# Kernel optimization log

Hardware: AMD Instinct MI355X
Metric: run time of the kernel (lower is better)

## Reference

```python
import jax, jax.numpy as jnp
import numpy as np

B, S, D, H = 4, 2048, 512, 8
KD = D // H          # key_dim == head_dim == 64
FFN = 4 * D

def _ln(x, g, b, eps):
    mu = x.mean(-1, keepdims=True)
    var = ((x - mu) ** 2).mean(-1, keepdims=True)
    return (x - mu) / jnp.sqrt(var + eps) * g + b

def setup_inputs():
    key = jax.random.key(0)
    ks = jax.random.split(key, 8)
    def lin(k, o, i, scale=0.02):
        k1, k2 = jax.random.split(k)
        return (jax.random.normal(k1, (o, i), jnp.float32) * scale,
                jax.random.normal(k2, (o,), jnp.float32) * scale)
    wq, bq = lin(ks[0], D, D)
    wk, bk = lin(ks[1], D, D)
    wv, bv = lin(ks[2], D, D)
    wg, bg = lin(ks[3], D, D)
    wo, bo = lin(ks[4], D, D)
    fc1_w, fc1_b = lin(ks[5], FFN, D)
    fc2_w, fc2_b = lin(ks[6], D, FFN)
    return {
        'src': jax.random.normal(ks[7], (B, S, D), jnp.float32),
        'mask': jnp.zeros((S, S), jnp.bool_),
        'padding_mask': jnp.zeros((B, S), jnp.bool_),
        'wq': wq, 'bq': bq, 'wk': wk, 'bk': bk, 'wv': wv, 'bv': bv,
        'wg': wg, 'bg': bg, 'wo': wo, 'bo': bo,
        'fc1_w': fc1_w, 'fc1_b': fc1_b, 'fc2_w': fc2_w, 'fc2_b': fc2_b,
        'ln_ffn_g': jnp.ones((FFN,), jnp.float32), 'ln_ffn_b': jnp.zeros((FFN,), jnp.float32),
        'n0_g': jnp.ones((D,), jnp.float32), 'n0_b': jnp.zeros((D,), jnp.float32),
        'n1_g': jnp.ones((D,), jnp.float32), 'n1_b': jnp.zeros((D,), jnp.float32),
    }

def reference(src, mask, padding_mask, wq, bq, wk, bk, wv, bv, wg, bg, wo, bo,
              fc1_w, fc1_b, fc2_w, fc2_b, ln_ffn_g, ln_ffn_b, n0_g, n0_b, n1_g, n1_b):
    b, s, d = src.shape
    # RetNet per-head decay mask (h, s, s): exp((i-j)*log(gamma_h)) on the lower triangle,
    # row-normalized by sqrt(row sum) (torchscale RetNetRelPos, parallel mode).
    idx = jnp.arange(s)
    diff = (idx[:, None] - idx[None, :]).astype(src.dtype)
    decay = jnp.log(1.0 - 2.0 ** (-5.0 - jnp.arange(H, dtype=src.dtype)))
    dm = jnp.where(diff[None] >= 0, jnp.exp(diff[None] * decay[:, None, None]), 0.0)
    dm = dm / jnp.sqrt(dm.sum(-1, keepdims=True))
    # projections; k scaled by key_dim**-0.5 before head split
    q = (src @ wq.T + bq).reshape(b, s, H, KD).transpose(0, 2, 1, 3)
    k = ((src @ wk.T + bk) * (KD ** -0.5)).reshape(b, s, H, KD).transpose(0, 2, 1, 3)
    v = src @ wv.T + bv
    g = src @ wg.T + bg
    # parallel retention: additive decay bias, detached L1 row normalization
    qk = jnp.einsum('bhid,bhjd->bhij', q, k) + dm[None]
    den = jnp.maximum(jnp.abs(jax.lax.stop_gradient(qk).sum(-1, keepdims=True)), 1.0)
    qk = qk / den
    vr = v.reshape(b, s, H, KD).transpose(0, 2, 1, 3)
    o = jnp.einsum('bhij,bhjd->bhid', qk, vr).transpose(0, 2, 1, 3)  # (b,s,h,hd)
    # per-head LayerNorm, eps=1e-6, no affine
    mu = o.mean(-1, keepdims=True)
    o = (o - mu) / jnp.sqrt(((o - mu) ** 2).mean(-1, keepdims=True) + 1e-6)
    o = jax.nn.silu(g) * o.reshape(b, s, d)
    o = o @ wo.T + bo
    # post-norm residual layout
    x = _ln(src + o, n0_g, n0_b, 1e-5)
    h = jax.nn.gelu(x @ fc1_w.T + fc1_b, approximate=False)
    h = _ln(h, ln_ffn_g, ln_ffn_b, 1e-6)  # subln
    h = h @ fc2_w.T + fc2_b
    return _ln(x + h, n1_g, n1_b, 1e-5)
```

## Files before the change

kernel.cpp:

```cpp
#include <hip/hip_runtime.h>
#include <hip/hip_bf16.h>
#include <math.h>

#define DEV __device__ __forceinline__

typedef __attribute__((ext_vector_type(4))) float f32x4;
typedef __attribute__((ext_vector_type(16))) float f32x16;
typedef __attribute__((ext_vector_type(8))) short bf16x8;
typedef __attribute__((ext_vector_type(8))) unsigned short u16x8;
typedef unsigned short u16;
typedef unsigned int u32;

DEV u16 f2bf(float f) {
  union { float f; u32 u; } v; v.f = f;
  u32 r = v.u + 0x7fffu + ((v.u >> 16) & 1u);
  return (u16)(r >> 16);
}
DEV float bf2f(u16 h) {
  union { u32 u; float f; } v; v.u = ((u32)h) << 16;
  return v.f;
}
DEV float bfel(bf16x8 v, int e) {
  union { bf16x8 b; u16x8 u; } x; x.b = v; return bf2f(x.u[e]);
}

DEV void gl_lds16(const u16* g, u16* s) {
  __builtin_amdgcn_global_load_lds((const __attribute__((address_space(1))) void*)g,
                                   (__attribute__((address_space(3))) void*)s, 16, 0, 0);
}

DEV void barrier_() {
  __builtin_amdgcn_sched_barrier(0);
  asm volatile("" ::: "memory");
  __builtin_amdgcn_s_barrier();
  asm volatile("" ::: "memory");
  __builtin_amdgcn_sched_barrier(0);
}

#define MFMA16(a, b, c) __builtin_amdgcn_mfma_f32_16x16x32_bf16((a), (b), (c), 0, 0, 0)
#define MFMA32(a, b, c) __builtin_amdgcn_mfma_f32_32x32x16_bf16((a), (b), (c), 0, 0, 0)

DEV void cast8(const float* in, u16* out, float s) {
  f32x4 a = *(const f32x4*)in;
  f32x4 b = *(const f32x4*)(in + 4);
  u16x8 r;
  r[0] = f2bf(a[0] * s); r[1] = f2bf(a[1] * s); r[2] = f2bf(a[2] * s); r[3] = f2bf(a[3] * s);
  r[4] = f2bf(b[0] * s); r[5] = f2bf(b[1] * s); r[6] = f2bf(b[2] * s); r[7] = f2bf(b[3] * s);
  *(u16x8*)out = r;
}

__global__ __launch_bounds__(256) void prep_cast(
    const float* __restrict__ src, const float* __restrict__ wq, const float* __restrict__ wk,
    const float* __restrict__ wv, const float* __restrict__ wg, const float* __restrict__ wo,
    const float* __restrict__ fc1, const float* __restrict__ fc2,
    const float* __restrict__ bq, const float* __restrict__ bk,
    const float* __restrict__ bv, const float* __restrict__ bg,
    u16* __restrict__ src_bf, u16* __restrict__ Wcat, u16* __restrict__ wo_bf,
    u16* __restrict__ fc1_bf, u16* __restrict__ fc2_bf, float* __restrict__ bcat) {
  int u = blockIdx.x * 256 + threadIdx.x;
  if (u < 524288) {
    cast8(src + (size_t)u * 8, src_bf + (size_t)u * 8, 1.0f);
  } else if (u < 557056) {
    int v = u - 524288; cast8(wq + (size_t)v * 8, Wcat + (size_t)v * 8, 1.0f);
  } else if (u < 589824) {
    int v = u - 557056; cast8(wk + (size_t)v * 8, Wcat + 262144 + (size_t)v * 8, 0.125f);
  } else if (u < 622592) {
    int v = u - 589824; cast8(wv + (size_t)v * 8, Wcat + 524288 + (size_t)v * 8, 1.0f);
  } else if (u < 655360) {
    int v = u - 622592; cast8(wg + (size_t)v * 8, Wcat + 786432 + (size_t)v * 8, 1.0f);
  } else if (u < 688128) {
    int v = u - 655360; cast8(wo + (size_t)v * 8, wo_bf + (size_t)v * 8, 1.0f);
  } else if (u < 819200) {
    int v = u - 688128; cast8(fc1 + (size_t)v * 8, fc1_bf + (size_t)v * 8, 1.0f);
  } else if (u < 950272) {
    int v = u - 819200; cast8(fc2 + (size_t)v * 8, fc2_bf + (size_t)v * 8, 1.0f);
  } else if (u < 950528) {
    int v = u - 950272;
    #pragma unroll
    for (int e = 0; e < 8; e++) {
      int c = v * 8 + e;
      float val;
      if (c < 512)       val = bq[c];
      else if (c < 1024) val = bk[c - 512] * 0.125f;
      else if (c < 1536) val = bv[c - 1024];
      else               val = bg[c - 1536];
      bcat[c] = val;
    }
  }
}

template <int ACT>
__global__ __launch_bounds__(256) void gemm_v3(
    const u16* __restrict__ A, const u16* __restrict__ W, const float* __restrict__ bias,
    u16* __restrict__ Ob, int N, int K, int TN) {
  __shared__ __align__(16) u16 sm[2][16384];
  const int t = threadIdx.x, l = t & 63;
  const int w = t >> 6, wr = (w >> 1) * 64, wc = (w & 1) * 64;
  const int lc = l & 15, lch = l >> 4;
  const int NT = K >> 6;

  const int orig = blockIdx.x;
  const int cpx = gridDim.x >> 3;
  const int sid = (orig & 7) * cpx + (orig >> 3);
  const int bm = (sid / TN) * 128, bn = (sid % TN) * 128;

  const int srow = t >> 3, sc8 = t & 7;
  const u16* stA = A + (size_t)(bm + srow) * K + ((sc8 ^ (srow & 7)) * 8);
  const u16* stB = W + (size_t)(bn + srow) * K + ((sc8 ^ (srow & 7)) * 8);

#define STAGE(bidx, kt)                                                        \
  {                                                                            \
    u16* d = (u16*)sm[bidx] + t * 8;                                           \
    _Pragma("unroll")                                                          \
    for (int j = 0; j < 4; j++)                                                \
      gl_lds16(stA + (size_t)j * 32 * K + (kt), d + j * 2048);                 \
    _Pragma("unroll")                                                          \
    for (int j = 0; j < 4; j++)                                                \
      gl_lds16(stB + (size_t)j * 32 * K + (kt), d + 8192 + j * 2048);          \
  }

  f32x4 acc[4][4] = {};

  STAGE(0, 0)

  for (int tt = 0; tt < NT; ++tt) {
    if (tt + 1 < NT) {
      STAGE((tt + 1) & 1, (tt + 1) * 64)
      asm volatile("s_waitcnt vmcnt(8)" ::: "memory");
    } else {
      asm volatile("s_waitcnt vmcnt(0)" ::: "memory");
    }
    barrier_();
    const u16* bufp = sm[tt & 1];
    bf16x8 af[4][2], bfv[4][2];
    #pragma unroll
    for (int mi = 0; mi < 4; mi++) {
      const int row = wr + mi * 16 + lc;
      #pragma unroll
      for (int ks = 0; ks < 2; ks++) {
        const int ch = ks * 4 + lch;
        af[mi][ks] = *(const bf16x8*)&bufp[row * 64 + ((ch ^ (row & 7)) * 8)];
      }
    }
    #pragma unroll
    for (int ni = 0; ni < 4; ni++) {
      const int row = wc + ni * 16 + lc;
      #pragma unroll
      for (int ks = 0; ks < 2; ks++) {
        const int ch = ks * 4 + lch;
        bfv[ni][ks] = *(const bf16x8*)&bufp[8192 + row * 64 + ((ch ^ (row & 7)) * 8)];
      }
    }
    #pragma unroll
    for (int ks = 0; ks < 2; ks++)
      #pragma unroll
      for (int mi = 0; mi < 4; mi++)
        #pragma unroll
        for (int ni = 0; ni < 4; ni++)
          acc[mi][ni] = MFMA16(af[mi][ks], bfv[ni][ks], acc[mi][ni]);
    asm volatile("s_waitcnt lgkmcnt(0)" ::: "memory");
    barrier_();
  }
#undef STAGE

  u16* osm = (u16*)sm;
  #pragma unroll
  for (int ni = 0; ni < 4; ni++) {
    const int col = wc + ni * 16 + lc;
    const float bb = bias[bn + col];
    const int ckey = col >> 3, clow = col & 7;
    #pragma unroll
    for (int mi = 0; mi < 4; mi++) {
      #pragma unroll
      for (int r = 0; r < 4; r++) {
        const int row = wr + mi * 16 + lch * 4 + r;
        float v = acc[mi][ni][r] + bb;
        if (ACT == 1) v = 0.5f * v * (1.0f + erff(v * 0.70710678118f));
        osm[row * 128 + ((ckey ^ ((row & 7) << 1)) << 3) + clow] = f2bf(v);
      }
    }
  }
  __syncthreads();
  #pragma unroll
  for (int p = 0; p < 8; p++) {
    const int flat = p * 256 + t;
    const int row = flat >> 4, c = flat & 15;
    u16x8 y = *(const u16x8*)&osm[row * 128 + ((c ^ ((row & 7) << 1)) << 3)];
    *(u16x8*)&Ob[(size_t)(bm + row) * N + bn + c * 8] = y;
  }
}

template <int ACT>
__global__ __launch_bounds__(256) void gemm_m64(
    const u16* __restrict__ A, const u16* __restrict__ W, const float* __restrict__ bias,
    u16* __restrict__ Ob, int N, int K, int TN) {
  __shared__ __align__(16) u16 sm[2][12288];
  const int t = threadIdx.x, l = t & 63;
  const int w = t >> 6, wr = (w >> 1) * 32, wc = (w & 1) * 64;
  const int lc = l & 15, lch = l >> 4;
  const int NT = K >> 6;

  const int orig = blockIdx.x;
  const int cpx = gridDim.x >> 3;
  const int sid = (orig & 7) * cpx + (orig >> 3);
  const int bm = (sid / TN) * 64, bn = (sid % TN) * 128;

  const int srow = t >> 3, sc8 = t & 7;
  const u16* stA = A + (size_t)(bm + srow) * K + ((sc8 ^ (srow & 7)) * 8);
  const u16* stB = W + (size_t)(bn + srow) * K + ((sc8 ^ (srow & 7)) * 8);

#define STAGE(bidx, kt)                                                        \
  {                                                                            \
    u16* d = (u16*)sm[bidx] + t * 8;                                           \
    _Pragma("unroll")                                                          \
    for (int j = 0; j < 2; j++)                                                \
      gl_lds16(stA + (size_t)j * 32 * K + (kt), d + j * 2048);                 \
    _Pragma("unroll")                                                          \
    for (int j = 0; j < 4; j++)                                                \
      gl_lds16(stB + (size_t)j * 32 * K + (kt), d + 4096 + j * 2048);          \
  }

  f32x4 acc[2][4] = {};

  STAGE(0, 0)

  for (int tt = 0; tt < NT; ++tt) {
    if (tt + 1 < NT) {
      STAGE((tt + 1) & 1, (tt + 1) * 64)
      asm volatile("s_waitcnt vmcnt(6)" ::: "memory");
    } else {
      asm volatile("s_waitcnt vmcnt(0)" ::: "memory");
    }
    barrier_();
    const u16* bufp = sm[tt & 1];
    bf16x8 af[2][2], bfv[4][2];
    #pragma unroll
    for (int mi = 0; mi < 2; mi++) {
      const int row = wr + mi * 16 + lc;
      #pragma unroll
      for (int ks = 0; ks < 2; ks++) {
        const int ch = ks * 4 + lch;
        af[mi][ks] = *(const bf16x8*)&bufp[row * 64 + ((ch ^ (row & 7)) * 8)];
      }
    }
    #pragma unroll
    for (int ni = 0; ni < 4; ni++) {
      const int row = wc + ni * 16 + lc;
      #pragma unroll
      for (int ks = 0; ks < 2; ks++) {
        const int ch = ks * 4 + lch;
        bfv[ni][ks] = *(const bf16x8*)&bufp[4096 + row * 64 + ((ch ^ (row & 7)) * 8)];
      }
    }
    #pragma unroll
    for (int ks = 0; ks < 2; ks++)
      #pragma unroll
      for (int mi = 0; mi < 2; mi++)
        #pragma unroll
        for (int ni = 0; ni < 4; ni++)
          acc[mi][ni] = MFMA16(af[mi][ks], bfv[ni][ks], acc[mi][ni]);
    asm volatile("s_waitcnt lgkmcnt(0)" ::: "memory");
    barrier_();
  }
#undef STAGE

  u16* osm = (u16*)sm;
  #pragma unroll
  for (int ni = 0; ni < 4; ni++) {
    const int col = wc + ni * 16 + lc;
    const float bb = bias[bn + col];
    const int ckey = col >> 3, clow = col & 7;
    #pragma unroll
    for (int mi = 0; mi < 2; mi++) {
      #pragma unroll
      for (int r = 0; r < 4; r++) {
        const int row = wr + mi * 16 + lch * 4 + r;
        float v = acc[mi][ni][r] + bb;
        if (ACT == 1) v = 0.5f * v * (1.0f + erff(v * 0.70710678118f));
        osm[row * 128 + ((ckey ^ ((row & 7) << 1)) << 3) + clow] = f2bf(v);
      }
    }
  }
  __syncthreads();
  #pragma unroll
  for (int p = 0; p < 4; p++) {
    const int flat = p * 256 + t;
    const int row = flat >> 4, c = flat & 15;
    u16x8 y = *(const u16x8*)&osm[row * 128 + ((c ^ ((row & 7) << 1)) << 3)];
    *(u16x8*)&Ob[(size_t)(bm + row) * N + bn + c * 8] = y;
  }
}

__global__ __launch_bounds__(256) void transkv(
    const u16* __restrict__ qkvg, u16* __restrict__ ktg, u16* __restrict__ vtg,
    float* __restrict__ Wtab) {
  __shared__ u16 Lk[64 * 72], Lv[64 * 72];
  const int t = threadIdx.x;
  const int bh = blockIdx.x, c = blockIdx.y, b = bh >> 3, h = bh & 7;
  const int jt = c * 64;
  const u16* kptr = qkvg + (size_t)(b * 2048 + jt) * 2048 + 512 + h * 64;
  const u16* vptr = kptr + 512;
  const int r0 = t >> 3, c0 = (t & 7) * 8;
  u16x8 k0 = *(const u16x8*)(kptr + (size_t)r0 * 2048 + c0);
  u16x8 k1 = *(const u16x8*)(kptr + (size_t)(r0 + 32) * 2048 + c0);
  u16x8 v0 = *(const u16x8*)(vptr + (size_t)r0 * 2048 + c0);
  u16x8 v1 = *(const u16x8*)(vptr + (size_t)(r0 + 32) * 2048 + c0);
  #pragma unroll
  for (int e = 0; e < 8; e++) {
    Lk[(c0 + e) * 72 + r0] = k0[e];  Lk[(c0 + e) * 72 + 32 + r0] = k1[e];
    Lv[(c0 + e) * 72 + r0] = v0[e];  Lv[(c0 + e) * 72 + 32 + r0] = v1[e];
  }
  __syncthreads();
  {
    u16* kd = ktg + (size_t)bh * 64 * 2048 + jt;
    u16* vd = vtg + (size_t)bh * 64 * 2048 + jt;
    *(u16x8*)(kd + (size_t)r0 * 2048 + c0)        = *(const u16x8*)&Lk[r0 * 72 + c0];
    *(u16x8*)(kd + (size_t)(r0 + 32) * 2048 + c0) = *(const u16x8*)&Lk[(r0 + 32) * 72 + c0];
    *(u16x8*)(vd + (size_t)r0 * 2048 + c0)        = *(const u16x8*)&Lv[r0 * 72 + c0];
    *(u16x8*)(vd + (size_t)(r0 + 32) * 2048 + c0) = *(const u16x8*)&Lv[(r0 + 32) * 72 + c0];
  }
  if (t < 64) {
    const float gamma = 1.0f - exp2f(-5.0f - (float)h);
    float acc = 0.0f, p = 1.0f;
    for (int jj = 0; jj < 64; jj++) {
      acc += p * bf2f(Lv[t * 72 + (63 - jj)]);
      p *= gamma;
    }
    Wtab[((size_t)bh * 32 + c) * 64 + t] = acc;
  }
}

__global__ __launch_bounds__(256) void scan_kernel(
    const u16* __restrict__ ktg, float* __restrict__ Ctab, float* __restrict__ ksum) {
  __shared__ float ps[4][64];
  const int t = threadIdx.x, bh = blockIdx.x, h = bh & 7;
  const int a = t & 63, q = t >> 6;
  const u16* kr = ktg + (size_t)bh * 64 * 2048 + (size_t)a * 2048 + q * 512;
  float s = 0.0f;
  for (int j = 0; j < 512; j += 8) {
    u16x8 v = *(const u16x8*)(kr + j);
    #pragma unroll
    for (int e = 0; e < 8; e++) s += bf2f(v[e]);
  }
  ps[q][a] = s;
  __syncthreads();
  if (t < 64) {
    ksum[bh * 64 + t] = ps[0][t] + ps[1][t] + ps[2][t] + ps[3][t];
    const float gamma = 1.0f - exp2f(-5.0f - (float)h);
    const float g64 = exp2f(64.0f * log2f(gamma));
    float* Wp = Ctab + (size_t)bh * 32 * 64 + t;
    float C = 0.0f;
    for (int c = 0; c < 32; c++) {
      C = C * g64 + Wp[c * 64];
      Wp[c * 64] = C;
    }
  }
}

__global__ __launch_bounds__(256) void vtk_kernel(
    const u16* __restrict__ vtg, const u16* __restrict__ ktg, u16* __restrict__ vtk) {
  __shared__ float red[3][4096];
  const int t = threadIdx.x, l = t & 63, w = t >> 6;
  const int bh = blockIdx.x;
  const int lc = l & 15, lch = l >> 4;
  const u16* vb = vtg + (size_t)bh * 64 * 2048;
  const u16* kb = ktg + (size_t)bh * 64 * 2048;
  f32x4 acc[4][4] = {};
  for (int it = 0; it < 16; ++it) {
    const int j0 = w * 512 + it * 32 + lch * 8;
    bf16x8 af[4], bfr[4];
    #pragma unroll
    for (int mt = 0; mt < 4; mt++)
      af[mt] = *(const bf16x8*)(vb + (size_t)(mt * 16 + lc) * 2048 + j0);
    #pragma unroll
    for (int nt = 0; nt < 4; nt++)
      bfr[nt] = *(const bf16x8*)(kb + (size_t)(nt * 16 + lc) * 2048 + j0);
    #pragma unroll
    for (int mt = 0; mt < 4; mt++)
      #pragma unroll
      for (int nt = 0; nt < 4; nt++)
        acc[mt][nt] = MFMA16(af[mt], bfr[nt], acc[mt][nt]);
  }
  if (w > 0) {
    #pragma unroll
    for (int mt = 0; mt < 4; mt++)
      #pragma unroll
      for (int nt = 0; nt < 4; nt++)
        #pragma unroll
        for (int r = 0; r < 4; r++)
          red[w - 1][(mt * 16 + lch * 4 + r) * 64 + nt * 16 + lc] = acc[mt][nt][r];
  }
  __syncthreads();
  if (w == 0) {
    u16* out = vtk + (size_t)bh * 64 * 64;
    #pragma unroll
    for (int mt = 0; mt < 4; mt++)
      #pragma unroll
      for (int nt = 0; nt < 4; nt++)
        #pragma unroll
        for (int r = 0; r < 4; r++) {
          int row = mt * 16 + lch * 4 + r, col = nt * 16 + lc;
          float v = acc[mt][nt][r] + red[0][row * 64 + col] + red[1][row * 64 + col] +
                    red[2][row * 64 + col];
          out[row * 64 + col] = f2bf(v);
        }
  }
}

__global__ __launch_bounds__(512) void ret_out(
    const u16* __restrict__ qkvg, const u16* __restrict__ vtg,
    const u16* __restrict__ vtk, const float* __restrict__ Ctab,
    const float* __restrict__ ksum, u16* __restrict__ gated) {
  const int S = 2048, DD = 2048;
  const int bh = blockIdx.x, b = bh >> 3, h = bh & 7;
  const int t = threadIdx.x, l = t & 63, w = t >> 6;
  const int lid = l & 31, hi = l >> 5;
  const int wrow = blockIdx.y * 256 + w * 32;
  const int i_q = wrow + lid;
  const int chunk = wrow >> 6;
  const int iloc = i_q & 63;

  __shared__ __align__(16) u16 sm[18432];
  float* smf = (float*)sm;

  const size_t base = (size_t)b * S * DD + (size_t)h * 64;
  const u16* qp = qkvg + base;
  const u16* gp = qkvg + base + 1536;

  const float gamma = 1.0f - exp2f(-5.0f - (float)h);
  const float l2g = log2f(gamma);
  const float rowsum = (1.0f - exp2f((float)(i_q + 1) * l2g)) * exp2f(5.0f + (float)h);
  const float rrs = rsqrtf(rowsum);

  {
    const int il = t >> 3, j0 = (t & 7) * 8;
    u16x8 row;
    #pragma unroll
    for (int e = 0; e < 8; e++) {
      int d = il - (j0 + e);
      row[e] = (d >= 0) ? f2bf(exp2f((float)d * l2g)) : (u16)0;
    }
    *(u16x8*)&sm[il * 72 + j0] = row;
  }
  if (t < 256) {
    int cc = blockIdx.y * 4 - 1 + (t >> 6);
    smf[4608 + t] = (cc >= 0) ? Ctab[((size_t)bh * 32 + cc) * 64 + (t & 63)] : 0.0f;
  } else if (t < 320) {
    smf[4864 + (t - 256)] = ksum[bh * 64 + (t - 256)];
  }
  __syncthreads();

  bf16x8 qf[4];
  #pragma unroll
  for (int kc = 0; kc < 4; kc++)
    qf[kc] = *(const bf16x8*)(qp + (size_t)i_q * DD + kc * 16 + 8 * hi);

  const u16* vt_b = vtg + (size_t)bh * 64 * S;
  const u16* vk_b = vtk + (size_t)bh * 64 * 64;

  f32x16 accO0, accO1;
  #pragma unroll
  for (int r = 0; r < 16; r++) { accO0[r] = 0.0f; accO1[r] = 0.0f; }

  #pragma unroll
  for (int kc = 0; kc < 4; kc++) {
    bf16x8 lb = *(const bf16x8*)&sm[iloc * 72 + kc * 16 + hi * 8];
    bf16x8 va0 = *(const bf16x8*)(vt_b + (size_t)lid * S + chunk * 64 + kc * 16 + hi * 8);
    bf16x8 va1 = *(const bf16x8*)(vt_b + (size_t)(lid + 32) * S + chunk * 64 + kc * 16 + hi * 8);
    accO0 = MFMA32(va0, lb, accO0);
    accO1 = MFMA32(va1, lb, accO1);
  }
  {
    const float gpw = exp2f((float)(iloc + 1) * l2g);
    const float* Cst = &smf[4608 + (w >> 1) * 64];
    #pragma unroll
    for (int r = 0; r < 16; r++) {
      int br = (r & 3) + 8 * (r >> 2) + 4 * hi;
      accO0[r] += gpw * Cst[br];
      accO1[r] += gpw * Cst[32 + br];
    }
  }
  #pragma unroll
  for (int r = 0; r < 16; r++) { accO0[r] *= rrs; accO1[r] *= rrs; }
  #pragma unroll
  for (int kc = 0; kc < 4; kc++) {
    bf16x8 ka0 = *(const bf16x8*)(vk_b + (size_t)lid * 64 + kc * 16 + hi * 8);
    bf16x8 ka1 = *(const bf16x8*)(vk_b + (size_t)(lid + 32) * 64 + kc * 16 + hi * 8);
    accO0 = MFMA32(ka0, qf[kc], accO0);
    accO1 = MFMA32(ka1, qf[kc], accO1);
  }
  float dsum = 0.0f;
  #pragma unroll
  for (int kc = 0; kc < 4; kc++) {
    const float* Ks = &smf[4864 + kc * 16 + hi * 8];
    #pragma unroll
    for (int e = 0; e < 8; e++) dsum += bfel(qf[kc], e) * Ks[e];
  }
  dsum += __shfl_xor(dsum, 32);
  float den = dsum + sqrtf(rowsum);
  float rden = 1.0f / fmaxf(fabsf(den), 1.0f);

  float o0[16], o1[16];
  float s1 = 0.0f, s2 = 0.0f;
  #pragma unroll
  for (int r = 0; r < 16; r++) {
    o0[r] = accO0[r] * rden; s1 += o0[r]; s2 += o0[r] * o0[r];
    o1[r] = accO1[r] * rden; s1 += o1[r]; s2 += o1[r] * o1[r];
  }
  s1 += __shfl_xor(s1, 32);
  s2 += __shfl_xor(s2, 32);
  float mu = s1 * (1.0f / 64.0f);
  float var = s2 * (1.0f / 64.0f) - mu * mu;
  float rv = rsqrtf(var + 1e-6f);

  __syncthreads();

  u16* Ot = sm + w * 2304;
  #pragma unroll
  for (int r = 0; r < 16; r++) {
    int d = (r & 3) + 8 * (r >> 2) + 4 * hi;
    Ot[lid * 72 + d]      = f2bf((o0[r] - mu) * rv);
    Ot[lid * 72 + 32 + d] = f2bf((o1[r] - mu) * rv);
  }
  {
    const int i2 = l >> 1, half = l & 1;
    const int row = wrow + i2;
    #pragma unroll
    for (int c = 0; c < 4; c++) {
      u16x8 y8 = *(const u16x8*)&Ot[i2 * 72 + half * 32 + c * 8];
      u16x8 g8 = *(const u16x8*)(gp + (size_t)row * DD + half * 32 + c * 8);
      u16x8 o8;
      #pragma unroll
      for (int e = 0; e < 8; e++) {
        float gv = bf2f(g8[e]);
        float sg = gv / (1.0f + __expf(-gv));
        o8[e] = f2bf(bf2f(y8[e]) * sg);
      }
      *(u16x8*)&gated[((size_t)(b * S + row)) * 512 + h * 64 + half * 32 + c * 8] = o8;
    }
  }
}

__global__ __launch_bounds__(256) void add_ln512(
    const float* __restrict__ A, const u16* __restrict__ Bv,
    const float* __restrict__ gam, const float* __restrict__ bet, float eps,
    float* __restrict__ Of, u16* __restrict__ Ob) {
  int row = blockIdx.x * 4 + (threadIdx.x >> 6);
  int l = threadIdx.x & 63;
  const float* a = A + (size_t)row * 512 + l * 8;
  f32x4 a0 = *(const f32x4*)a, a1 = *(const f32x4*)(a + 4);
  u16x8 cv = *(const u16x8*)(Bv + (size_t)row * 512 + l * 8);
  float x[8];
  #pragma unroll
  for (int e = 0; e < 4; e++) { x[e] = a0[e] + bf2f(cv[e]); x[4 + e] = a1[e] + bf2f(cv[4 + e]); }
  float s = 0.f, s2 = 0.f;
  #pragma unroll
  for (int e = 0; e < 8; e++) { s += x[e]; s2 += x[e] * x[e]; }
  #pragma unroll
  for (int m = 1; m <= 32; m <<= 1) { s += __shfl_xor(s, m); s2 += __shfl_xor(s2, m); }
  float mu = s * (1.0f / 512.0f);
  float var = s2 * (1.0f / 512.0f) - mu * mu;
  float rinv = rsqrtf(var + eps);
  f32x4 g0 = *(const f32x4*)(gam + l * 8), g1 = *(const f32x4*)(gam + l * 8 + 4);
  f32x4 b0 = *(const f32x4*)(bet + l * 8), b1 = *(const f32x4*)(bet + l * 8 + 4);
  f32x4 y0, y1;
  #pragma unroll
  for (int e = 0; e < 4; e++) {
    y0[e] = (x[e] - mu) * rinv * g0[e] + b0[e];
    y1[e] = (x[4 + e] - mu) * rinv * g1[e] + b1[e];
  }
  float* op = Of + (size_t)row * 512 + l * 8;
  *(f32x4*)op = y0;
  *(f32x4*)(op + 4) = y1;
  if (Ob) {
    u16x8 rb_;
    #pragma unroll
    for (int e = 0; e < 4; e++) { rb_[e] = f2bf(y0[e]); rb_[4 + e] = f2bf(y1[e]); }
    *(u16x8*)(Ob + (size_t)row * 512 + l * 8) = rb_;
  }
}

__global__ __launch_bounds__(256) void subln_ffn(
    u16* __restrict__ hbuf, const float* __restrict__ gam, const float* __restrict__ bet) {
  int row = blockIdx.x * 4 + (threadIdx.x >> 6);
  int l = threadIdx.x & 63;
  u16* p = hbuf + (size_t)row * 2048;
  float x[32];
  #pragma unroll
  for (int cch = 0; cch < 4; cch++) {
    u16x8 v = *(const u16x8*)(p + cch * 512 + l * 8);
    #pragma unroll
    for (int e = 0; e < 8; e++) x[cch * 8 + e] = bf2f(v[e]);
  }
  float s = 0.f, s2 = 0.f;
  #pragma unroll
  for (int e = 0; e < 32; e++) { s += x[e]; s2 += x[e] * x[e]; }
  #pragma unroll
  for (int m = 1; m <= 32; m <<= 1) { s += __shfl_xor(s, m); s2 += __shfl_xor(s2, m); }
  float mu = s * (1.0f / 2048.0f);
  float var = s2 * (1.0f / 2048.0f) - mu * mu;
  float rinv = rsqrtf(var + 1e-6f);
  #pragma unroll
  for (int cch = 0; cch < 4; cch++) {
    int col = cch * 512 + l * 8;
    f32x4 g0 = *(const f32x4*)(gam + col), g1 = *(const f32x4*)(gam + col + 4);
    f32x4 b0 = *(const f32x4*)(bet + col), b1 = *(const f32x4*)(bet + col + 4);
    u16x8 o;
    #pragma unroll
    for (int e = 0; e < 4; e++) {
      o[e]     = f2bf((x[cch * 8 + e]     - mu) * rinv * g0[e] + b0[e]);
      o[4 + e] = f2bf((x[cch * 8 + 4 + e] - mu) * rinv * g1[e] + b1[e]);
    }
    *(u16x8*)(p + col) = o;
  }
}

extern "C" void kernel_launch(void* const* d_in, const int* in_sizes, int n_in,
                              void* d_out, int out_size, void* d_ws, size_t ws_size,
                              hipStream_t stream) {
  const float* src  = (const float*)d_in[0];
  const float* wq   = (const float*)d_in[3];
  const float* bq   = (const float*)d_in[4];
  const float* wk   = (const float*)d_in[5];
  const float* bk   = (const float*)d_in[6];
  const float* wv   = (const float*)d_in[7];
  const float* bv   = (const float*)d_in[8];
  const float* wg   = (const float*)d_in[9];
  const float* bg   = (const float*)d_in[10];
  const float* wo   = (const float*)d_in[11];
  const float* bo   = (const float*)d_in[12];
  const float* fc1w = (const float*)d_in[13];
  const float* fc1b = (const float*)d_in[14];
  const float* fc2w = (const float*)d_in[15];
  const float* fc2b = (const float*)d_in[16];
  const float* lng  = (const float*)d_in[17];
  const float* lnb  = (const float*)d_in[18];
  const float* n0g  = (const float*)d_in[19];
  const float* n0b  = (const float*)d_in[20];
  const float* n1g  = (const float*)d_in[21];
  const float* n1b  = (const float*)d_in[22];

  if (ws_size < 91242496u) return;

  char* ws = (char*)d_ws;
  u16*   src_bf = (u16*)(ws + 0);
  u16*   Wcat   = (u16*)(ws + 8388608);
  u16*   wo_bf  = (u16*)(ws + 10485760);
  u16*   fc1_bf = (u16*)(ws + 11010048);
  u16*   fc2_bf = (u16*)(ws + 13107200);
  float* bcat   = (float*)(ws + 15204352);
  u16*   qkvg   = (u16*)(ws + 15212544);
  u16*   gated  = (u16*)(ws + 48766976);
  u16*   attn   = (u16*)(ws + 57155584);
  float* xf     = (float*)(ws + 65544192);
  u16*   vtg    = (u16*)(ws + 65544192);
  u16*   ktg    = (u16*)(ws + 73932800);
  u16*   xbf    = (u16*)(ws + 82321408);
  float* Ctab   = (float*)(ws + 90710016);
  u16*   vtkb   = (u16*)(ws + 90972160);
  float* ksumb  = (float*)(ws + 91234304);

  prep_cast<<<3713, 256, 0, stream>>>(src, wq, wk, wv, wg, wo, fc1w, fc2w,
                                      bq, bk, bv, bg,
                                      src_bf, Wcat, wo_bf, fc1_bf, fc2_bf, bcat);
  gemm_v3<0><<<1024, 256, 0, stream>>>(src_bf, Wcat, bcat, qkvg, 2048, 512, 16);
  transkv<<<dim3(32, 32), 256, 0, stream>>>(qkvg, ktg, vtg, Ctab);
  scan_kernel<<<32, 256, 0, stream>>>(ktg, Ctab, ksumb);
  vtk_kernel<<<32, 256, 0, stream>>>(vtg, ktg, vtkb);
  ret_out<<<dim3(32, 8), 512, 0, stream>>>(qkvg, vtg, vtkb, Ctab, ksumb, gated);
  gemm_m64<0><<<512, 256, 0, stream>>>(gated, wo_bf, bo, attn, 512, 512, 4);
  add_ln512<<<2048, 256, 0, stream>>>(src, attn, n0g, n0b, 1e-5f, xf, xbf);
  gemm_v3<1><<<1024, 256, 0, stream>>>(xbf, fc1_bf, fc1b, qkvg, 2048, 512, 16);
  subln_ffn<<<2048, 256, 0, stream>>>(qkvg, lng, lnb);
  gemm_m64<0><<<512, 256, 0, stream>>>(qkvg, fc2_bf, fc2b, attn, 512, 2048, 4);
  add_ln512<<<2048, 256, 0, stream>>>(xf, attn, n1g, n1b, 1e-5f, (float*)d_out, nullptr);
}
```

Measured before the change: 183.9 us.

## Halve GEMM K-tile to 32 with smaller LDS, drop fp32 residual buffer

Both GEMM kernels now stage K in steps of 32 instead of 64, with a new 4-chunk XOR swizzle and half the shared-memory footprint per stage. This is meant to raise occupancy, at the cost of twice as many barriers per K loop. The residual for the final LayerNorm now reads the bf16 copy of x rather than an fp32 copy, so the first LN no longer writes fp32. That saves memory traffic but lowers the precision of the residual path.

After: 187.8 us. 2.1% more time.

```diff
diff --git a/kernel.cpp b/kernel.cpp
--- a/kernel.cpp
+++ b/kernel.cpp
@@ -90,80 +90,66 @@
 }
 
 template <int ACT>
-__global__ __launch_bounds__(256) void gemm_v3(
+__global__ __launch_bounds__(256) void gemm_v4(
     const u16* __restrict__ A, const u16* __restrict__ W, const float* __restrict__ bias,
     u16* __restrict__ Ob, int N, int K, int TN) {
-  __shared__ __align__(16) u16 sm[2][16384];
+  __shared__ __align__(16) u16 sm[16384];
   const int t = threadIdx.x, l = t & 63;
   const int w = t >> 6, wr = (w >> 1) * 64, wc = (w & 1) * 64;
   const int lc = l & 15, lch = l >> 4;
-  const int NT = K >> 6;
+  const int NT = K >> 5;
 
   const int orig = blockIdx.x;
   const int cpx = gridDim.x >> 3;
   const int sid = (orig & 7) * cpx + (orig >> 3);
   const int bm = (sid / TN) * 128, bn = (sid % TN) * 128;
 
-  const int srow = t >> 3, sc8 = t & 7;
-  const u16* stA = A + (size_t)(bm + srow) * K + ((sc8 ^ (srow & 7)) * 8);
-  const u16* stB = W + (size_t)(bn + srow) * K + ((sc8 ^ (srow & 7)) * 8);
-
-#define STAGE(bidx, kt)                                                        \
-  {                                                                            \
-    u16* d = (u16*)sm[bidx] + t * 8;                                           \
-    _Pragma("unroll")                                                          \
-    for (int j = 0; j < 4; j++)                                                \
-      gl_lds16(stA + (size_t)j * 32 * K + (kt), d + j * 2048);                 \
-    _Pragma("unroll")                                                          \
-    for (int j = 0; j < 4; j++)                                                \
-      gl_lds16(stB + (size_t)j * 32 * K + (kt), d + 8192 + j * 2048);          \
+  const int srow = t >> 2, sc = t & 3;
+  const int soff = (sc ^ ((srow >> 1) & 3)) * 8;
+  const u16* stA = A + (size_t)(bm + srow) * K + soff;
+  const u16* stB = W + (size_t)(bn + srow) * K + soff;
+  const size_t rstep = (size_t)64 * K;
+
+#define STAGE(bidx, kt)                                   \
+  {                                                       \
+    u16* d = sm + (bidx) * 8192 + t * 8;                  \
+    gl_lds16(stA + (kt), d);                              \
+    gl_lds16(stA + rstep + (kt), d + 2048);               \
+    gl_lds16(stB + (kt), d + 4096);                       \
+    gl_lds16(stB + rstep + (kt), d + 6144);               \
   }
 
   f32x4 acc[4][4] = {};
-
   STAGE(0, 0)
 
+  const int key = (lch ^ ((lc >> 1) & 3)) * 8;
   for (int tt = 0; tt < NT; ++tt) {
     if (tt + 1 < NT) {
-      STAGE((tt + 1) & 1, (tt + 1) * 64)
-      asm volatile("s_waitcnt vmcnt(8)" ::: "memory");
+      STAGE((tt + 1) & 1, (tt + 1) * 32)
+      asm volatile("s_waitcnt vmcnt(4)" ::: "memory");
     } else {
       asm volatile("s_waitcnt vmcnt(0)" ::: "memory");
     }
     barrier_();
-    const u16* bufp = sm[tt & 1];
-    bf16x8 af[4][2], bfv[4][2];
-    #pragma unroll
-    for (int mi = 0; mi < 4; mi++) {
-      const int row = wr + mi * 16 + lc;
-      #pragma unroll
-      for (int ks = 0; ks < 2; ks++) {
-        const int ch = ks * 4 + lch;
-        af[mi][ks] = *(const bf16x8*)&bufp[row * 64 + ((ch ^ (row & 7)) * 8)];
-      }
-    }
-    #pragma unroll
-    for (int ni = 0; ni < 4; ni++) {
-      const int row = wc + ni * 16 + lc;
-      #pragma unroll
-      for (int ks = 0; ks < 2; ks++) {
-        const int ch = ks * 4 + lch;
-        bfv[ni][ks] = *(const bf16x8*)&bufp[8192 + row * 64 + ((ch ^ (row & 7)) * 8)];
-      }
-    }
-    #pragma unroll
-    for (int ks = 0; ks < 2; ks++)
-      #pragma unroll
-      for (int mi = 0; mi < 4; mi++)
-        #pragma unroll
-        for (int ni = 0; ni < 4; ni++)
-          acc[mi][ni] = MFMA16(af[mi][ks], bfv[ni][ks], acc[mi][ni]);
+    const u16* bufp = sm + (tt & 1) * 8192;
+    bf16x8 af[4], bfv[4];
+    #pragma unroll
+    for (int mi = 0; mi < 4; mi++)
+      af[mi] = *(const bf16x8*)&bufp[(wr + mi * 16 + lc) * 32 + key];
+    #pragma unroll
+    for (int ni = 0; ni < 4; ni++)
+      bfv[ni] = *(const bf16x8*)&bufp[4096 + (wc + ni * 16 + lc) * 32 + key];
+    #pragma unroll
+    for (int mi = 0; mi < 4; mi++)
+      #pragma unroll
+      for (int ni = 0; ni < 4; ni++)
+        acc[mi][ni] = MFMA16(af[mi], bfv[ni], acc[mi][ni]);
     asm volatile("s_waitcnt lgkmcnt(0)" ::: "memory");
     barrier_();
   }
 #undef STAGE
 
-  u16* osm = (u16*)sm;
+  u16* osm = sm;
   #pragma unroll
   for (int ni = 0; ni < 4; ni++) {
     const int col = wc + ni * 16 + lc;
@@ -191,80 +177,65 @@
 }
 
 template <int ACT>
-__global__ __launch_bounds__(256) void gemm_m64(
+__global__ __launch_bounds__(256) void gemm_m64_v4(
     const u16* __restrict__ A, const u16* __restrict__ W, const float* __restrict__ bias,
     u16* __restrict__ Ob, int N, int K, int TN) {
-  __shared__ __align__(16) u16 sm[2][12288];
+  __shared__ __align__(16) u16 sm[12288];
   const int t = threadIdx.x, l = t & 63;
   const int w = t >> 6, wr = (w >> 1) * 32, wc = (w & 1) * 64;
   const int lc = l & 15, lch = l >> 4;
-  const int NT = K >> 6;
+  const int NT = K >> 5;
 
   const int orig = blockIdx.x;
   const int cpx = gridDim.x >> 3;
   const int sid = (orig & 7) * cpx + (orig >> 3);
   const int bm = (sid / TN) * 64, bn = (sid % TN) * 128;
 
-  const int srow = t >> 3, sc8 = t & 7;
-  const u16* stA = A + (size_t)(bm + srow) * K + ((sc8 ^ (srow & 7)) * 8);
-  const u16* stB = W + (size_t)(bn + srow) * K + ((sc8 ^ (srow & 7)) * 8);
-
-#define STAGE(bidx, kt)                                                        \
-  {                                                                            \
-    u16* d = (u16*)sm[bidx] + t * 8;                                           \
-    _Pragma("unroll")                                                          \
-    for (int j = 0; j < 2; j++)                                                \
-      gl_lds16(stA + (size_t)j * 32 * K + (kt), d + j * 2048);                 \
-    _Pragma("unroll")                                                          \
-    for (int j = 0; j < 4; j++)                                                \
-      gl_lds16(stB + (size_t)j * 32 * K + (kt), d + 4096 + j * 2048);          \
+  const int srow = t >> 2, sc = t & 3;
+  const int soff = (sc ^ ((srow >> 1) & 3)) * 8;
+  const u16* stA = A + (size_t)(bm + srow) * K + soff;
+  const u16* stB = W + (size_t)(bn + srow) * K + soff;
+  const size_t rstep = (size_t)64 * K;
+
+#define STAGE(bidx, kt)                                   \
+  {                                                       \
+    u16* d = sm + (bidx) * 6144 + t * 8;                  \
+    gl_lds16(stA + (kt), d);                              \
+    gl_lds16(stB + (kt), d + 2048);                       \
+    gl_lds16(stB + rstep + (kt), d + 4096);               \
   }
 
   f32x4 acc[2][4] = {};
-
   STAGE(0, 0)
 
+  const int key = (lch ^ ((lc >> 1) & 3)) * 8;
   for (int tt = 0; tt < NT; ++tt) {
     if (tt + 1 < NT) {
-      STAGE((tt + 1) & 1, (tt + 1) * 64)
-      asm volatile("s_waitcnt vmcnt(6)" ::: "memory");
+      STAGE((tt + 1) & 1, (tt + 1) * 32)
+      asm volatile("s_waitcnt vmcnt(3)" ::: "memory");
     } else {
       asm volatile("s_waitcnt vmcnt(0)" ::: "memory");
     }
     barrier_();
-    const u16* bufp = sm[tt & 1];
-    bf16x8 af[2][2], bfv[4][2];
-    #pragma unroll
-    for (int mi = 0; mi < 2; mi++) {
-      const int row = wr + mi * 16 + lc;
-      #pragma unroll
-      for (int ks = 0; ks < 2; ks++) {
-        const int ch = ks * 4 + lch;
-        af[mi][ks] = *(const bf16x8*)&bufp[row * 64 + ((ch ^ (row & 7)) * 8)];
-      }
-    }
-    #pragma unroll
-    for (int ni = 0; ni < 4; ni++) {
-      const int row = wc + ni * 16 + lc;
-      #pragma unroll
-      for (int ks = 0; ks < 2; ks++) {
-        const int ch = ks * 4 + lch;
-        bfv[ni][ks] = *(const bf16x8*)&bufp[4096 + row * 64 + ((ch ^ (row & 7)) * 8)];
-      }
-    }
-    #pragma unroll
-    for (int ks = 0; ks < 2; ks++)
-      #pragma unroll
-      for (int mi = 0; mi < 2; mi++)
-        #pragma unroll
-        for (int ni = 0; ni < 4; ni++)
-          acc[mi][ni] = MFMA16(af[mi][ks], bfv[ni][ks], acc[mi][ni]);
+    const u16* bufp = sm + (tt & 1) * 6144;
+    bf16x8 af[2], bfv[4];
+    #pragma unroll
+    for (int mi = 0; mi < 2; mi++)
+      af[mi] = *(const bf16x8*)&bufp[(wr + mi * 16 + lc) * 32 + key];
+    #pragma unroll
+    for (int ni = 0; ni < 4; ni++)
+      bfv[ni] = *(const bf16x8*)&bufp[2048 + (wc + ni * 16 + lc) * 32 + key];
+    #pragma unroll
+    for (int mi = 0; mi < 2; mi++)
+      #pragma unroll
+      for (int ni = 0; ni < 4; ni++)
+        acc[mi][ni] = MFMA16(af[mi], bfv[ni], acc[mi][ni]);
     asm volatile("s_waitcnt lgkmcnt(0)" ::: "memory");
     barrier_();
   }
 #undef STAGE
 
-  u16* osm = (u16*)sm;
+  u16* osm = sm;
   #pragma unroll
   for (int ni = 0; ni < 4; ni++) {
     const int col = wc + ni * 16 + lc;
@@ -541,18 +512,25 @@
   }
 }
 
-__global__ __launch_bounds__(256) void add_ln512(
-    const float* __restrict__ A, const u16* __restrict__ Bv,
+template <int AF32, int WF>
+__global__ __launch_bounds__(256) void add_lnT(
+    const void* __restrict__ Ap, const u16* __restrict__ Bv,
     const float* __restrict__ gam, const float* __restrict__ bet, float eps,
     float* __restrict__ Of, u16* __restrict__ Ob) {
   int row = blockIdx.x * 4 + (threadIdx.x >> 6);
   int l = threadIdx.x & 63;
-  const float* a = A + (size_t)row * 512 + l * 8;
-  f32x4 a0 = *(const f32x4*)a, a1 = *(const f32x4*)(a + 4);
+  float x[8];
   u16x8 cv = *(const u16x8*)(Bv + (size_t)row * 512 + l * 8);
-  float x[8];
-  #pragma unroll
-  for (int e = 0; e < 4; e++) { x[e] = a0[e] + bf2f(cv[e]); x[4 + e] = a1[e] + bf2f(cv[4 + e]); }
+  if (AF32) {
+    const float* a = (const float*)Ap + (size_t)row * 512 + l * 8;
+    f32x4 a0 = *(const f32x4*)a, a1 = *(const f32x4*)(a + 4);
+    #pragma unroll
+    for (int e = 0; e < 4; e++) { x[e] = a0[e] + bf2f(cv[e]); x[4 + e] = a1[e] + bf2f(cv[4 + e]); }
+  } else {
+    u16x8 av = *(const u16x8*)((const u16*)Ap + (size_t)row * 512 + l * 8);
+    #pragma unroll
+    for (int e = 0; e < 8; e++) x[e] = bf2f(av[e]) + bf2f(cv[e]);
+  }
   float s = 0.f, s2 = 0.f;
   #pragma unroll
   for (int e = 0; e < 8; e++) { s += x[e]; s2 += x[e] * x[e]; }
@@ -569,9 +547,11 @@
     y0[e] = (x[e] - mu) * rinv * g0[e] + b0[e];
     y1[e] = (x[4 + e] - mu) * rinv * g1[e] + b1[e];
   }
-  float* op = Of + (size_t)row * 512 + l * 8;
-  *(f32x4*)op = y0;
-  *(f32x4*)(op + 4) = y1;
+  if (WF) {
+    float* op = Of + (size_t)row * 512 + l * 8;
+    *(f32x4*)op = y0;
+    *(f32x4*)(op + 4) = y1;
+  }
   if (Ob) {
     u16x8 rb_;
     #pragma unroll
@@ -652,7 +632,6 @@
   u16*   qkvg   = (u16*)(ws + 15212544);
   u16*   gated  = (u16*)(ws + 48766976);
   u16*   attn   = (u16*)(ws + 57155584);
-  float* xf     = (float*)(ws + 65544192);
   u16*   vtg    = (u16*)(ws + 65544192);
   u16*   ktg    = (u16*)(ws + 73932800);
   u16*   xbf    = (u16*)(ws + 82321408);
@@ -663,15 +642,15 @@
   prep_cast<<<3713, 256, 0, stream>>>(src, wq, wk, wv, wg, wo, fc1w, fc2w,
                                       bq, bk, bv, bg,
                                       src_bf, Wcat, wo_bf, fc1_bf, fc2_bf, bcat);
-  gemm_v3<0><<<1024, 256, 0, stream>>>(src_bf, Wcat, bcat, qkvg, 2048, 512, 16);
+  gemm_v4<0><<<1024, 256, 0, stream>>>(src_bf, Wcat, bcat, qkvg, 2048, 512, 16);
   transkv<<<dim3(32, 32), 256, 0, stream>>>(qkvg, ktg, vtg, Ctab);
   scan_kernel<<<32, 256, 0, stream>>>(ktg, Ctab, ksumb);
   vtk_kernel<<<32, 256, 0, stream>>>(vtg, ktg, vtkb);
   ret_out<<<dim3(32, 8), 512, 0, stream>>>(qkvg, vtg, vtkb, Ctab, ksumb, gated);
-  gemm_m64<0><<<512, 256, 0, stream>>>(gated, wo_bf, bo, attn, 512, 512, 4);
-  add_ln512<<<2048, 256, 0, stream>>>(src, attn, n0g, n0b, 1e-5f, xf, xbf);
-  gemm_v3<1><<<1024, 256, 0, stream>>>(xbf, fc1_bf, fc1b, qkvg, 2048, 512, 16);
+  gemm_m64_v4<0><<<512, 256, 0, stream>>>(gated, wo_bf, bo, attn, 512, 512, 4);
+  add_lnT<1, 0><<<2048, 256, 0, stream>>>(src, attn, n0g, n0b, 1e-5f, nullptr, xbf);
+  gemm_v4<1><<<1024, 256, 0, stream>>>(xbf, fc1_bf, fc1b, qkvg, 2048, 512, 16);
   subln_ffn<<<2048, 256, 0, stream>>>(qkvg, lng, lnb);
-  gemm_m64<0><<<512, 256, 0, stream>>>(qkvg, fc2_bf, fc2b, attn, 512, 2048, 4);
-  add_ln512<<<2048, 256, 0, stream>>>(xf, attn, n1g, n1b, 1e-5f, (float*)d_out, nullptr);
-}
+  gemm_m64_v4<0><<<512, 256, 0, stream>>>(qkvg, fc2_bf, fc2b, attn, 512, 2048, 4);
+  add_lnT<0, 1><<<2048, 256, 0, stream>>>(xbf, attn, n1g, n1b, 1e-5f, (float*)d_out, nullptr);
+}
```
